# Optimization experiments

Measured on AMD Instinct MI355X. Metric: run time of the kernel, lower is better.

## Reference

```python
import jax, jax.numpy as jnp
import numpy as np

EPS_LN = 1e-5

def _layernorm(x, g, b):
    mu = x.mean(-1, keepdims=True)
    var = ((x - mu) ** 2).mean(-1, keepdims=True)
    return (x - mu) / jnp.sqrt(var + EPS_LN) * g + b


def setup_inputs() -> dict:
    key = jax.random.key(0)
    B, N, D, H = 4, 2048, 256, 4
    hid = int(D * 2.0)
    ks = jax.random.split(key, 12)
    x = jax.random.normal(ks[0], (B, N, D), jnp.float32)
    Au = jax.random.uniform(ks[1], (N, N)) < 0.004
    A = jnp.logical_or(Au, Au.T)
    A = A.at[jnp.arange(N), jnp.arange(N)].set(False)
    Af = A.astype(jnp.float32)
    deg = Af.sum(axis=1)
    L = jnp.diag(deg) - Af                      # graph Laplacian (N,N), PSD
    adjacency = Af + jnp.eye(N, dtype=jnp.float32)  # self loops so no empty softmax rows
    s = lambda k, sh, f: jax.random.normal(k, sh, jnp.float32) * f
    sc = 1.0 / np.sqrt(D)
    Wc = s(ks[2], (D, D), sc); bc = jnp.zeros((D,), jnp.float32)
    Wq = s(ks[3], (D, D), sc); Wk = s(ks[4], (D, D), sc); Wv = s(ks[5], (D, D), sc)
    Wo = s(ks[6], (D, D), sc); bo = jnp.zeros((D,), jnp.float32)
    W1 = s(ks[7], (D, hid), sc); b1 = jnp.zeros((hid,), jnp.float32)
    W2 = s(ks[8], (hid, D), 1.0 / np.sqrt(hid)); b2 = jnp.zeros((D,), jnp.float32)
    g1 = jnp.ones((D,), jnp.float32); be1 = jnp.zeros((D,), jnp.float32)
    g2 = jnp.ones((D,), jnp.float32); be2 = jnp.zeros((D,), jnp.float32)
    g3 = jnp.ones((D,), jnp.float32); be3 = jnp.zeros((D,), jnp.float32)
    return dict(x=x, L=L, adjacency=adjacency, Wc=Wc, bc=bc, g1=g1, be1=be1,
                Wq=Wq, Wk=Wk, Wv=Wv, Wo=Wo, bo=bo, g2=g2, be2=be2,
                W1=W1, b1=b1, W2=W2, b2=b2, g3=g3, be3=be3)


def reference(x, L, adjacency, Wc, bc, g1, be1, Wq, Wk, Wv, Wo, bo,
              g2, be2, W1, b1, W2, b2, g3, be3):
    B, N, D = x.shape
    H = 4
    hd = D // H
    # --- LaplacianConv: normalize L to eigenvalues in [-1, 1] ---
    eig = jnp.linalg.eigvalsh(L)               # ascending
    lam_max = eig[-1] + 1e-8
    L_norm = 2.0 * L / lam_max - jnp.eye(N, dtype=L.dtype)
    # per-channel matmul in torch == single propagation L_norm @ x
    xp = jnp.einsum('mn,bnf->bmf', L_norm, x)
    h = xp @ Wc + bc
    h = _layernorm(h, g1, be1)
    h = jax.nn.relu(h)
    x1 = h + x                                  # residual (in_dim == out_dim)
    # --- adjacency-masked multi-head attention ---
    q = (x1 @ Wq).reshape(B, N, H, hd).transpose(0, 2, 1, 3)  # (B,H,N,hd)
    k = (x1 @ Wk).reshape(B, N, H, hd).transpose(0, 2, 1, 3)
    v = (x1 @ Wv).reshape(B, N, H, hd).transpose(0, 2, 1, 3)
    scores = jnp.einsum('bhnd,bhmd->bhnm', q, k) / np.sqrt(hd).astype(np.float32)
    scores = jnp.where(adjacency[None, None] > 0, scores, jnp.float32(-1e9))
    attn = jax.nn.softmax(scores, axis=-1)
    o = jnp.einsum('bhnm,bhmd->bhnd', attn, v)
    o = o.transpose(0, 2, 1, 3).reshape(B, N, D)
    o = o @ Wo + bo
    x2 = _layernorm(x1 + o, g2, be2)
    # --- MLP ---
    m = jax.nn.gelu(x2 @ W1 + b1, approximate=False) @ W2 + b2
    return _layernorm(x2 + m, g3, be3)
```

## Files before the change

### kernel.cpp

```cpp
#include <hip/hip_runtime.h>
#include <math.h>

typedef __bf16 bf16;
typedef bf16 bf16x8 __attribute__((ext_vector_type(8)));
typedef float f32x4 __attribute__((ext_vector_type(4)));

#define LDS_PAD 40
#define SENT 2048
#define LANCZOS_M 12

__global__ __launch_bounds__(256) void k_pre(
    const float* __restrict__ Wc, const float* __restrict__ Wq, const float* __restrict__ Wk,
    const float* __restrict__ Wv, const float* __restrict__ Wo, const float* __restrict__ W1,
    const float* __restrict__ W2, const float* __restrict__ x, const float* __restrict__ adj,
    bf16* __restrict__ WcT, bf16* __restrict__ WqT, bf16* __restrict__ WkT,
    bf16* __restrict__ WvT, bf16* __restrict__ WoT, bf16* __restrict__ W1T,
    bf16* __restrict__ W2T, bf16* __restrict__ xT,
    int* __restrict__ cnt, unsigned short* __restrict__ cols)
{
    __shared__ float tile[32][33];
    int z = blockIdx.z;
    if (z == 11) {
        int flat = blockIdx.y * 16 + blockIdx.x;
        if (flat >= 512) return;
        int row = flat * 4 + (threadIdx.x >> 6);
        int lane = threadIdx.x & 63;
        int base = 0;
        for (int c0 = 0; c0 < 2048; c0 += 64) {
            float a = adj[(long)row * 2048 + c0 + lane];
            unsigned long long m = __ballot(a != 0.0f);
            if (a != 0.0f) {
                int pos = base + __popcll(m & ((1ull << lane) - 1ull));
                if (pos < 64) cols[(long)row * 64 + pos] = (unsigned short)(c0 + lane);
            }
            base += __popcll(m);
        }
        int c = base < 64 ? base : 64;
        if (lane >= c) cols[(long)row * 64 + lane] = (unsigned short)SENT;
        if (lane == 0) cnt[row] = c;
        return;
    }
    const float* src; bf16* dst; int R, C;
    switch (z) {
        case 0: src = Wc; dst = WcT; R = 256; C = 256; break;
        case 1: src = Wq; dst = WqT; R = 256; C = 256; break;
        case 2: src = Wk; dst = WkT; R = 256; C = 256; break;
        case 3: src = Wv; dst = WvT; R = 256; C = 256; break;
        case 4: src = Wo; dst = WoT; R = 256; C = 256; break;
        case 5: src = W1; dst = W1T; R = 256; C = 512; break;
        case 6: src = W2; dst = W2T; R = 512; C = 256; break;
        default: {
            int b = z - 7;
            src = x + (long)b * 2048 * 256; dst = xT + (long)b * 256 * 2048;
            R = 2048; C = 256;
        }
    }
    int c0 = blockIdx.x * 32, r0 = blockIdx.y * 32;
    if (c0 >= C || r0 >= R) return;
    int tx = threadIdx.x & 31, ty = threadIdx.x >> 5;
#pragma unroll
    for (int j = 0; j < 4; ++j)
        tile[ty + 8 * j][tx] = src[(long)(r0 + ty + 8 * j) * C + c0 + tx];
    __syncthreads();
#pragma unroll
    for (int j = 0; j < 4; ++j)
        dst[(long)(c0 + ty + 8 * j) * R + r0 + tx] = (bf16)tile[tx][ty + 8 * j];
}

__global__ __launch_bounds__(1024) void k_main(
    const int* __restrict__ cnt, const unsigned short* __restrict__ cols, float* __restrict__ lamOut,
    const float* __restrict__ L, const bf16* __restrict__ xT, float* __restrict__ xp0f)
{
    __shared__ float va[2064], vb[2064];
    __shared__ float redf[16], redf2[16];
    __shared__ int   redi[16];
    __shared__ float bcast, bcast2;
    __shared__ float alphaA[LANCZOS_M], betaA[LANCZOS_M];
    __shared__ bf16 As[64 * LDS_PAD];
    __shared__ bf16 Bs[256 * LDS_PAD];

    int t = threadIdx.x;
    if (blockIdx.x != 0) {
        int bx = blockIdx.x - 1;
        int rowBlk = (bx & 31) * 64;
        int z  = (bx >> 5) & 3;
        int ks = bx >> 7;
        long kbase = (long)ks * 1024;
        const bf16* BT = xT + (long)z * 256 * 2048;
        int w = t >> 6, lane = t & 63;
        int q = lane >> 4, l15 = lane & 15;
        int wm = w & 3, wn = w >> 2;

        f32x4 acc[4];
#pragma unroll
        for (int i = 0; i < 4; ++i) acc[i] = (f32x4){0.0f, 0.0f, 0.0f, 0.0f};

        int ar = t >> 4, ac = (t & 15) * 2;
        int br = t >> 2, bc = (t & 3) * 8;
        const float* Ap = L + (long)(rowBlk + ar) * 2048 + kbase + ac;
        const bf16* Bp = BT + (long)br * 2048 + kbase + bc;
        float2 fA = *(const float2*)Ap;
        uint4  rB = *(const uint4*)Bp;
        for (int kt = 0; kt < 1024; kt += 32) {
            __syncthreads();
            {
                union { bf16 h[2]; unsigned u; } pk;
                pk.h[0] = (bf16)fA.x; pk.h[1] = (bf16)fA.y;
                *(unsigned*)&As[ar * LDS_PAD + ac] = pk.u;
            }
            *(uint4*)&Bs[br * LDS_PAD + bc] = rB;
            __syncthreads();
            if (kt + 32 < 1024) {
                fA = *(const float2*)(Ap + kt + 32);
                rB = *(const uint4*)(Bp + kt + 32);
            }
            bf16x8 a = *(const bf16x8*)&As[(wm * 16 + l15) * LDS_PAD + q * 8];
#pragma unroll
            for (int nt = 0; nt < 4; ++nt) {
                bf16x8 b = *(const bf16x8*)&Bs[((wn * 4 + nt) * 16 + l15) * LDS_PAD + q * 8];
                acc[nt] = __builtin_amdgcn_mfma_f32_16x16x32_bf16(a, b, acc[nt], 0, 0, 0);
            }
        }
        long zRow = (long)ks * 8192 + (long)z * 2048 + rowBlk + wm * 16 + q * 4;
#pragma unroll
        for (int nt = 0; nt < 4; ++nt) {
            int col = (wn * 4 + nt) * 16 + l15;
#pragma unroll
            for (int r = 0; r < 4; ++r)
                xp0f[(zRow + r) * 256 + col] = acc[nt][r];
        }
        return;
    }
    int wid = t >> 6, lane = t & 63;
    int r0 = t, r1 = t + 1024;
    int c0 = cnt[r0], c1 = cnt[r1];
    int p0 = (c0 + 7) & ~7, p1 = (c1 + 7) & ~7;

    uint4 cr0[8], cr1[8];
#pragma unroll
    for (int j = 0; j < 8; ++j) {
        cr0[j] = ((const uint4*)(cols + (long)r0 * 64))[j];
        cr1[j] = ((const uint4*)(cols + (long)r1 * 64))[j];
    }

    int md = max(c0, c1);
#pragma unroll
    for (int off = 32; off >= 1; off >>= 1) md = max(md, __shfl_xor(md, off));
    if (lane == 0) redi[wid] = md;
    __syncthreads();
    if (t == 0) {
        int m = 0;
        for (int i = 0; i < 16; ++i) m = max(m, redi[i]);
        bcast = (float)(2 * (m - 1)) + 1.0f;
    }
    for (int i = t; i < 2048; i += 1024) {
        unsigned u = (unsigned)i * 2654435761u;
        u ^= u >> 16; u *= 2246822519u; u ^= u >> 13;
        float mag = 0.5f + (float)((u >> 9) & 1023) * (1.0f / 1024.0f);
        va[i] = (u & 1) ? mag : -mag;
    }
    if (t == 0) { va[SENT] = 0.0f; vb[SENT] = 0.0f; }
    __syncthreads();
    float hiBound = bcast;

    float d0 = va[r0], d1 = va[r1];
    float pz = d0 * d0 + d1 * d1;
#pragma unroll
    for (int off = 32; off >= 1; off >>= 1) pz += __shfl_xor(pz, off);
    if (lane == 0) redf[wid] = pz;
    __syncthreads();
    if (t == 0) { float s = 0; for (int i = 0; i < 16; ++i) s += redf[i]; bcast = s; }
    __syncthreads();
    float sc = rsqrtf(fmaxf(bcast, 1e-30f));
    d0 *= sc; d1 *= sc;
    va[r0] = d0; va[r1] = d1;
    __syncthreads();

    float* cur = va; float* nxt = vb;
    float bp = 0.0f;
    float p0r = 0.0f, p1r = 0.0f;
    for (int it = 0; it < LANCZOS_M; ++it) {
        float sum0 = 0.0f, sum1 = 0.0f;
#pragma unroll
        for (int j = 0; j < 8; ++j)
            if (j * 8 < p0) {
                uint4 q = cr0[j];
                sum0 += cur[q.x & 0xffff] + cur[q.x >> 16] + cur[q.y & 0xffff] + cur[q.y >> 16]
                      + cur[q.z & 0xffff] + cur[q.z >> 16] + cur[q.w & 0xffff] + cur[q.w >> 16];
            }
#pragma unroll
        for (int j = 0; j < 8; ++j)
            if (j * 8 < p1) {
                uint4 q = cr1[j];
                sum1 += cur[q.x & 0xffff] + cur[q.x >> 16] + cur[q.y & 0xffff] + cur[q.y >> 16]
                      + cur[q.z & 0xffff] + cur[q.z >> 16] + cur[q.w & 0xffff] + cur[q.w >> 16];
            }
        float u0 = (float)c0 * d0 - sum0 - bp * p0r;
        float u1 = (float)c1 * d1 - sum1 - bp * p1r;
        float puv = u0 * d0 + u1 * d1;
        float puu = u0 * u0 + u1 * u1;
#pragma unroll
        for (int off = 32; off >= 1; off >>= 1) {
            puv += __shfl_xor(puv, off);
            puu += __shfl_xor(puu, off);
        }
        if (lane == 0) { redf[wid] = puv; redf2[wid] = puu; }
        __syncthreads();
        if (t == 0) {
            float sv = 0, su = 0;
            for (int i = 0; i < 16; ++i) { sv += redf[i]; su += redf2[i]; }
            float b = sqrtf(fmaxf(su - sv * sv, 1e-24f));
            alphaA[it] = sv; betaA[it] = b;
            bcast = sv; bcast2 = b;
        }
        __syncthreads();
        float alpha = bcast, beta = bcast2;
        float invb = 1.0f / beta;
        float w0 = u0 - alpha * d0, w1 = u1 - alpha * d1;
        p0r = d0; p1r = d1;
        d0 = w0 * invb; d1 = w1 * invb;
        nxt[r0] = d0; nxt[r1] = d1;
        __syncthreads();
        bp = beta;
        float* tmp = cur; cur = nxt; nxt = tmp;
    }

    if (t < 64) {
        float aa[LANCZOS_M], b2[LANCZOS_M];
#pragma unroll
        for (int i = 0; i < LANCZOS_M; ++i) { aa[i] = alphaA[i]; b2[i] = betaA[i] * betaA[i]; }
        float lo = 0.0f, hi = hiBound;
        for (int round = 0; round < 4; ++round) {
            float step = (hi - lo) * (1.0f / 65.0f);
            float xm = lo + step * (float)(lane + 1);
            float dd = aa[0] - xm;
            int neg = dd < 0.0f ? 1 : 0;
#pragma unroll
            for (int i = 1; i < LANCZOS_M; ++i) {
                float ad = fmaxf(fabsf(dd), 1e-12f);
                dd = (dd < 0.0f) ? -ad : ad;
                dd = aa[i] - xm - b2[i - 1] / dd;
                neg += dd < 0.0f ? 1 : 0;
            }
            unsigned long long mb = __ballot(neg >= LANCZOS_M);
            if (mb == 0ull) {
                lo = lo + step * 64.0f;
            } else {
                int fl = (int)(__ffsll((long long)mb) - 1);
                hi = lo + step * (float)(fl + 1);
                lo = lo + step * (float)fl;
            }
        }
        if (lane == 0) lamOut[0] = 0.5f * (lo + hi) + 1e-8f;
    }
}

template <int TA, int EPI>
__global__ __launch_bounds__(256) void k_gemm(
    const bf16* __restrict__ A0, const float* __restrict__ Apa, const float* __restrict__ Apb,
    const float* __restrict__ Aaux, const bf16* __restrict__ BTg,
    float* __restrict__ outF, bf16* __restrict__ outB,
    const float* __restrict__ bias, const float* __restrict__ resid,
    const float* __restrict__ gam, const float* __restrict__ bet,
    const float* __restrict__ lamPtr,
    int K, long aZ, long btZ, long outZrows, int ldOut)
{
    __shared__ bf16 As[32 * LDS_PAD];
    __shared__ bf16 Bs[256 * LDS_PAD];
    __shared__ float sL[2][32], sqL[2][32];

    int tid = threadIdx.x;
    int w = tid >> 6, lane = tid & 63;
    int q = lane >> 4, l15 = lane & 15;
    int wm = w & 1, wn = w >> 1;
    int rowBlk = blockIdx.x * 32;
    int colB = blockIdx.y * 256;
    const bf16* BT = BTg + (long)blockIdx.z * btZ + (long)blockIdx.y * 256 * (long)K;

    float s2 = 0.0f;
    if (TA == 2) s2 = 2.0f / lamPtr[0];

    f32x4 acc[8];
#pragma unroll
    for (int i = 0; i < 8; ++i) acc[i] = (f32x4){0.0f, 0.0f, 0.0f, 0.0f};

    int ar = tid >> 3, ac = (tid & 7) * 4;
    long abase = (long)(rowBlk + ar) * K + ac;
    const bf16* A = A0 + (long)blockIdx.z * aZ;
    const bf16* Bp = BT + (long)tid * K;

    uint2 aR;
    float4 pa0, pb0, xa0;
    uint4 bR0, bR1, bR2, bR3;
    if (TA == 1) {
        aR = *(const uint2*)(A + abase);
    } else {
        pa0 = *(const float4*)(Apa + abase);
        pb0 = *(const float4*)(Apb + abase);
        xa0 = *(const float4*)(Aaux + abase);
    }
    bR0 = ((const uint4*)Bp)[0]; bR1 = ((const uint4*)Bp)[1];
    bR2 = ((const uint4*)Bp)[2]; bR3 = ((const uint4*)Bp)[3];

    for (int kt = 0; kt < K; kt += 32) {
        __syncthreads();
        if (TA == 1) {
            *(uint2*)&As[ar * LDS_PAD + ac] = aR;
        } else {
            float pa[4] = {pa0.x, pa0.y, pa0.z, pa0.w};
            float pb[4] = {pb0.x, pb0.y, pb0.z, pb0.w};
            float xa[4] = {xa0.x, xa0.y, xa0.z, xa0.w};
            union { bf16 h[4]; uint2 u; } pk;
#pragma unroll
            for (int j = 0; j < 4; ++j) pk.h[j] = (bf16)(s2 * (pa[j] + pb[j]) - xa[j]);
            *(uint2*)&As[ar * LDS_PAD + ac] = pk.u;
        }
        {
            bf16* d = &Bs[tid * LDS_PAD];
            *(uint4*)(d + 0)  = bR0;
            *(uint4*)(d + 8)  = bR1;
            *(uint4*)(d + 16) = bR2;
            *(uint4*)(d + 24) = bR3;
        }
        __syncthreads();
        if (kt + 32 < K) {
            long nb = abase + kt + 32;
            if (TA == 1) {
                aR = *(const uint2*)(A + nb);
            } else {
                pa0 = *(const float4*)(Apa + nb);
                pb0 = *(const float4*)(Apb + nb);
                xa0 = *(const float4*)(Aaux + nb);
            }
            const bf16* p = Bp + kt + 32;
            bR0 = ((const uint4*)p)[0]; bR1 = ((const uint4*)p)[1];
            bR2 = ((const uint4*)p)[2]; bR3 = ((const uint4*)p)[3];
        }
        bf16x8 a = *(const bf16x8*)&As[(wm * 16 + l15) * LDS_PAD + q * 8];
#pragma unroll
        for (int nt = 0; nt < 8; ++nt) {
            bf16x8 b = *(const bf16x8*)&Bs[((wn * 8 + nt) * 16 + l15) * LDS_PAD + q * 8];
            acc[nt] = __builtin_amdgcn_mfma_f32_16x16x32_bf16(a, b, acc[nt], 0, 0, 0);
        }
    }

    long zRow = (long)blockIdx.z * outZrows + rowBlk + wm * 16 + q * 4;

    if (EPI == 0) {
#pragma unroll
        for (int nt = 0; nt < 8; ++nt) {
            int col = colB + (wn * 8 + nt) * 16 + l15;
#pragma unroll
            for (int r = 0; r < 4; ++r)
                outB[(zRow + r) * (long)ldOut + col] = (bf16)acc[nt][r];
        }
        return;
    }
    if (EPI == 3) {
#pragma unroll
        for (int nt = 0; nt < 8; ++nt) {
            int col = colB + (wn * 8 + nt) * 16 + l15;
            float bi = bias[col];
#pragma unroll
            for (int r = 0; r < 4; ++r) {
                float v = acc[nt][r] + bi;
                float g = 0.5f * v * (1.0f + erff(v * 0.70710678118654752440f));
                outB[(zRow + r) * (long)ldOut + col] = (bf16)g;
            }
        }
        return;
    }
    float s[4] = {0, 0, 0, 0}, sq[4] = {0, 0, 0, 0};
#pragma unroll
    for (int nt = 0; nt < 8; ++nt) {
        int col = colB + (wn * 8 + nt) * 16 + l15;
        float bi = bias[col];
#pragma unroll
        for (int r = 0; r < 4; ++r) {
            float v = acc[nt][r] + bi;
            if (EPI == 2) v += resid[(zRow + r) * 256 + col];
            acc[nt][r] = v;
            s[r] += v; sq[r] += v * v;
        }
    }
#pragma unroll
    for (int off = 1; off <= 8; off <<= 1) {
#pragma unroll
        for (int r = 0; r < 4; ++r) { s[r] += __shfl_xor(s[r], off); sq[r] += __shfl_xor(sq[r], off); }
    }
    if (l15 == 0) {
#pragma unroll
        for (int r = 0; r < 4; ++r) {
            sL[wn][wm * 16 + q * 4 + r] = s[r];
            sqL[wn][wm * 16 + q * 4 + r] = sq[r];
        }
    }
    __syncthreads();
    float mean[4], rstd[4];
#pragma unroll
    for (int r = 0; r < 4; ++r) {
        int row = wm * 16 + q * 4 + r;
        float st = sL[0][row] + sL[1][row];
        float sqt = sqL[0][row] + sqL[1][row];
        mean[r] = st * (1.0f / 256.0f);
        float var = sqt * (1.0f / 256.0f) - mean[r] * mean[r];
        rstd[r] = rsqrtf(var + 1e-5f);
    }
#pragma unroll
    for (int nt = 0; nt < 8; ++nt) {
        int col = colB + (wn * 8 + nt) * 16 + l15;
        float gc = gam[col], bc2 = bet[col];
#pragma unroll
        for (int r = 0; r < 4; ++r) {
            float v = (acc[nt][r] - mean[r]) * rstd[r] * gc + bc2;
            if (EPI == 1) v = fmaxf(v, 0.0f) + resid[(zRow + r) * 256 + col];
            long oi = (zRow + r) * (long)ldOut + col;
            outF[oi] = v;
            if (outB) outB[oi] = (bf16)v;
        }
    }
}

__global__ __launch_bounds__(256) void k_attn(const bf16* __restrict__ qg, const bf16* __restrict__ kg,
                                              const bf16* __restrict__ vg, bf16* __restrict__ og,
                                              const int* __restrict__ cnt, const unsigned short* __restrict__ cols)
{
    __shared__ unsigned short sc[64];
    __shared__ float sp[4][64];
    int row = blockIdx.x;
    int b = row >> 11, i = row & 2047;
    int tid = threadIdx.x, h = tid >> 6, lane = tid & 63;
    int c = cnt[i];
    if (tid < 64) sc[tid] = cols[(long)i * 64 + tid];
    __syncthreads();
    long qoff = (long)row * 256 + h * 64 + lane;
    float qd = (float)qg[qoff];
    long kvBase = (long)b * 2048;
    for (int j = 0; j < c; ++j) {
        int col = sc[j];
        float kd = (float)kg[(kvBase + col) * 256 + h * 64 + lane];
        float p = qd * kd;
#pragma unroll
        for (int off = 32; off >= 1; off >>= 1) p += __shfl_xor(p, off);
        if (lane == 0) sp[h][j] = p * 0.125f;
    }
    __syncthreads();
    float sj = (lane < c) ? sp[h][lane] : -3.0e38f;
    float mx = sj;
#pragma unroll
    for (int off = 32; off >= 1; off >>= 1) mx = fmaxf(mx, __shfl_xor(mx, off));
    float e = (lane < c) ? __expf(sj - mx) : 0.0f;
    float ssum = e;
#pragma unroll
    for (int off = 32; off >= 1; off >>= 1) ssum += __shfl_xor(ssum, off);
    if (lane < c) sp[h][lane] = e / ssum;
    __syncthreads();
    float acc = 0.0f;
    for (int j = 0; j < c; ++j) {
        int col = sc[j];
        acc += sp[h][j] * (float)vg[(kvBase + col) * 256 + h * 64 + lane];
    }
    og[qoff] = (bf16)acc;
}

extern "C" void kernel_launch(void* const* d_in, const int* in_sizes, int n_in,
                              void* d_out, int out_size, void* d_ws, size_t ws_size,
                              hipStream_t stream)
{
    const float* x   = (const float*)d_in[0];
    const float* L   = (const float*)d_in[1];
    const float* adj = (const float*)d_in[2];
    const float* Wc  = (const float*)d_in[3];
    const float* bc  = (const float*)d_in[4];
    const float* g1  = (const float*)d_in[5];
    const float* be1 = (const float*)d_in[6];
    const float* Wq  = (const float*)d_in[7];
    const float* Wk  = (const float*)d_in[8];
    const float* Wv  = (const float*)d_in[9];
    const float* Wo  = (const float*)d_in[10];
    const float* bo  = (const float*)d_in[11];
    const float* g2  = (const float*)d_in[12];
    const float* be2 = (const float*)d_in[13];
    const float* W1  = (const float*)d_in[14];
    const float* b1  = (const float*)d_in[15];
    const float* W2  = (const float*)d_in[16];
    const float* b2  = (const float*)d_in[17];
    const float* g3  = (const float*)d_in[18];
    const float* be3 = (const float*)d_in[19];
    float* out = (float*)d_out;

    char* ws = (char*)d_ws;
    size_t off = 0;
    auto alloc = [&](size_t bytes) -> void* {
        void* p = ws + off;
        off = (off + bytes + 255) & ~(size_t)255;
        return p;
    };
    float* lam           = (float*)alloc(256);
    int* cnt             = (int*)alloc(2048 * 4);
    unsigned short* cols = (unsigned short*)alloc(2048 * 64 * 2);
    bf16* WcT = (bf16*)alloc(65536 * 2);
    bf16* WqT = (bf16*)alloc(65536 * 2);
    bf16* WkT = (bf16*)alloc(65536 * 2);
    bf16* WvT = (bf16*)alloc(65536 * 2);
    bf16* WoT = (bf16*)alloc(65536 * 2);
    bf16* W1T = (bf16*)alloc(131072 * 2);
    bf16* W2T = (bf16*)alloc(131072 * 2);
    bf16* xT  = (bf16*)alloc((size_t)4 * 256 * 2048 * 2);
    float* xp0f = (float*)alloc((size_t)2 * 8192 * 256 * 4);
    float* x1f = (float*)alloc((size_t)8192 * 256 * 4);
    bf16* x1b  = (bf16*)alloc((size_t)8192 * 256 * 2);
    bf16* qb   = (bf16*)alloc((size_t)3 * 8192 * 256 * 2);
    bf16* ob   = (bf16*)alloc((size_t)8192 * 256 * 2);
    float* x2f = (float*)alloc((size_t)8192 * 256 * 4);
    bf16* x2b  = (bf16*)alloc((size_t)8192 * 256 * 2);
    bf16* m1   = (bf16*)alloc((size_t)8192 * 512 * 2);
    (void)in_sizes; (void)n_in; (void)out_size; (void)ws_size;

    dim3 blk(256);
    k_pre<<<dim3(16, 64, 12), blk, 0, stream>>>(Wc, Wq, Wk, Wv, Wo, W1, W2, x, adj,
                                                WcT, WqT, WkT, WvT, WoT, W1T, W2T, xT, cnt, cols);
    k_main<<<dim3(257), dim3(1024), 0, stream>>>(cnt, cols, lam, L, xT, xp0f);
    k_gemm<2, 1><<<dim3(256, 1, 1), blk, 0, stream>>>(
        nullptr, xp0f, xp0f + (size_t)8192 * 256, x, WcT, x1f, x1b, bc, x, g1, be1, lam,
        256, 0L, 0L, 0L, 256);
    k_gemm<1, 0><<<dim3(256, 1, 3), blk, 0, stream>>>(
        x1b, nullptr, nullptr, nullptr, WqT, nullptr, qb, nullptr, nullptr, nullptr, nullptr, nullptr,
        256, 0L, 65536L, 8192L, 256);
    bf16* kb  = qb + (size_t)8192 * 256;
    bf16* vb2 = qb + (size_t)2 * 8192 * 256;
    k_attn<<<dim3(8192), blk, 0, stream>>>(qb, kb, vb2, ob, cnt, cols);
    k_gemm<1, 2><<<dim3(256, 1, 1), blk, 0, stream>>>(
        ob, nullptr, nullptr, nullptr, WoT, x2f, x2b, bo, x1f, g2, be2, nullptr,
        256, 0L, 0L, 0L, 256);
    k_gemm<1, 3><<<dim3(256, 2, 1), blk, 0, stream>>>(
        x2b, nullptr, nullptr, nullptr, W1T, nullptr, m1, b1, nullptr, nullptr, nullptr, nullptr,
        256, 0L, 0L, 0L, 512);
    k_gemm<1, 2><<<dim3(256, 1, 1), blk, 0, stream>>>(
        m1, nullptr, nullptr, nullptr, W2T, out, nullptr, b2, x2f, g3, be3, nullptr,
        512, 0L, 0L, 0L, 256);
}
```

Measured before the change: 368.5 us.

## Fuse GEMM chains into two kernels keeping intermediates in LDS

Replaces the generic templated GEMM launches with two fused kernels. The first computes the Laplacian-conv GEMM with LayerNorm, ReLU and residual, then runs the Q/K/V projections from an LDS-resident x1 tile. The second chains the output projection with LayerNorm, W1 with GELU, and W2 with the final LayerNorm, keeping x2 and the MLP hidden tile in LDS. This removes four launches and the global round-trips for x1b, x2f/x2b and m1. In exchange, the grid for the QKV and W1 stages shrinks from 768/512 blocks to 256, each block does its GEMMs serially, and larger LDS use may lower occupancy.

```diff
diff --git a/kernel.cpp b/kernel.cpp
--- a/kernel.cpp
+++ b/kernel.cpp
@@ -8,6 +8,8 @@
 #define LDS_PAD 40
 #define SENT 2048
 #define LANCZOS_M 12
+#define X1P 264
+#define M1P 520
 
 __global__ __launch_bounds__(256) void k_pre(
     const float* __restrict__ Wc, const float* __restrict__ Wq, const float* __restrict__ Wk,
@@ -255,18 +257,15 @@
     }
 }
 
-template <int TA, int EPI>
-__global__ __launch_bounds__(256) void k_gemm(
-    const bf16* __restrict__ A0, const float* __restrict__ Apa, const float* __restrict__ Apb,
-    const float* __restrict__ Aaux, const bf16* __restrict__ BTg,
-    float* __restrict__ outF, bf16* __restrict__ outB,
-    const float* __restrict__ bias, const float* __restrict__ resid,
-    const float* __restrict__ gam, const float* __restrict__ bet,
-    const float* __restrict__ lamPtr,
-    int K, long aZ, long btZ, long outZrows, int ldOut)
+__global__ __launch_bounds__(256) void k_x1qkv(
+    const float* __restrict__ Apa, const float* __restrict__ Apb, const float* __restrict__ xg,
+    const bf16* __restrict__ WcT, const bf16* __restrict__ WqkvT,
+    const float* __restrict__ bcv, const float* __restrict__ gam, const float* __restrict__ bet,
+    const float* __restrict__ lamPtr, float* __restrict__ x1f, bf16* __restrict__ qkv)
 {
     __shared__ bf16 As[32 * LDS_PAD];
     __shared__ bf16 Bs[256 * LDS_PAD];
+    __shared__ bf16 x1t[32 * X1P];
     __shared__ float sL[2][32], sqL[2][32];
 
     int tid = threadIdx.x;
@@ -274,39 +273,25 @@
     int q = lane >> 4, l15 = lane & 15;
     int wm = w & 1, wn = w >> 1;
     int rowBlk = blockIdx.x * 32;
-    int colB = blockIdx.y * 256;
-    const bf16* BT = BTg + (long)blockIdx.z * btZ + (long)blockIdx.y * 256 * (long)K;
-
-    float s2 = 0.0f;
-    if (TA == 2) s2 = 2.0f / lamPtr[0];
+    float s2 = 2.0f / lamPtr[0];
 
     f32x4 acc[8];
 #pragma unroll
     for (int i = 0; i < 8; ++i) acc[i] = (f32x4){0.0f, 0.0f, 0.0f, 0.0f};
 
     int ar = tid >> 3, ac = (tid & 7) * 4;
-    long abase = (long)(rowBlk + ar) * K + ac;
-    const bf16* A = A0 + (long)blockIdx.z * aZ;
-    const bf16* Bp = BT + (long)tid * K;
-
-    uint2 aR;
-    float4 pa0, pb0, xa0;
-    uint4 bR0, bR1, bR2, bR3;
-    if (TA == 1) {
-        aR = *(const uint2*)(A + abase);
-    } else {
-        pa0 = *(const float4*)(Apa + abase);
-        pb0 = *(const float4*)(Apb + abase);
-        xa0 = *(const float4*)(Aaux + abase);
-    }
-    bR0 = ((const uint4*)Bp)[0]; bR1 = ((const uint4*)Bp)[1];
-    bR2 = ((const uint4*)Bp)[2]; bR3 = ((const uint4*)Bp)[3];
-
-    for (int kt = 0; kt < K; kt += 32) {
-        __syncthreads();
-        if (TA == 1) {
-            *(uint2*)&As[ar * LDS_PAD + ac] = aR;
-        } else {
+    long abase = (long)(rowBlk + ar) * 256 + ac;
+    const bf16* Bp = WcT + (long)tid * 256;
+
+    float4 pa0 = *(const float4*)(Apa + abase);
+    float4 pb0 = *(const float4*)(Apb + abase);
+    float4 xa0 = *(const float4*)(xg + abase);
+    uint4 bR0 = ((const uint4*)Bp)[0], bR1 = ((const uint4*)Bp)[1];
+    uint4 bR2 = ((const uint4*)Bp)[2], bR3 = ((const uint4*)Bp)[3];
+
+    for (int kt = 0; kt < 256; kt += 32) {
+        __syncthreads();
+        {
             float pa[4] = {pa0.x, pa0.y, pa0.z, pa0.w};
             float pb[4] = {pb0.x, pb0.y, pb0.z, pb0.w};
             float xa[4] = {xa0.x, xa0.y, xa0.z, xa0.w};
@@ -323,15 +308,11 @@
             *(uint4*)(d + 24) = bR3;
         }
         __syncthreads();
-        if (kt + 32 < K) {
+        if (kt + 32 < 256) {
             long nb = abase + kt + 32;
-            if (TA == 1) {
-                aR = *(const uint2*)(A + nb);
-            } else {
-                pa0 = *(const float4*)(Apa + nb);
-                pb0 = *(const float4*)(Apb + nb);
-                xa0 = *(const float4*)(Aaux + nb);
-            }
+            pa0 = *(const float4*)(Apa + nb);
+            pb0 = *(const float4*)(Apb + nb);
+            xa0 = *(const float4*)(xg + nb);
             const bf16* p = Bp + kt + 32;
             bR0 = ((const uint4*)p)[0]; bR1 = ((const uint4*)p)[1];
             bR2 = ((const uint4*)p)[2]; bR3 = ((const uint4*)p)[3];
@@ -344,41 +325,15 @@
         }
     }
 
-    long zRow = (long)blockIdx.z * outZrows + rowBlk + wm * 16 + q * 4;
-
-    if (EPI == 0) {
-#pragma unroll
-        for (int nt = 0; nt < 8; ++nt) {
-            int col = colB + (wn * 8 + nt) * 16 + l15;
-#pragma unroll
-            for (int r = 0; r < 4; ++r)
-                outB[(zRow + r) * (long)ldOut + col] = (bf16)acc[nt][r];
-        }
-        return;
-    }
-    if (EPI == 3) {
-#pragma unroll
-        for (int nt = 0; nt < 8; ++nt) {
-            int col = colB + (wn * 8 + nt) * 16 + l15;
-            float bi = bias[col];
-#pragma unroll
-            for (int r = 0; r < 4; ++r) {
-                float v = acc[nt][r] + bi;
-                float g = 0.5f * v * (1.0f + erff(v * 0.70710678118654752440f));
-                outB[(zRow + r) * (long)ldOut + col] = (bf16)g;
-            }
-        }
-        return;
-    }
+    long zRow = (long)rowBlk + wm * 16 + q * 4;
     float s[4] = {0, 0, 0, 0}, sq[4] = {0, 0, 0, 0};
 #pragma unroll
     for (int nt = 0; nt < 8; ++nt) {
-        int col = colB + (wn * 8 + nt) * 16 + l15;
-        float bi = bias[col];
+        int col = (wn * 8 + nt) * 16 + l15;
+        float bi = bcv[col];
 #pragma unroll
         for (int r = 0; r < 4; ++r) {
             float v = acc[nt][r] + bi;
-            if (EPI == 2) v += resid[(zRow + r) * 256 + col];
             acc[nt][r] = v;
             s[r] += v; sq[r] += v * v;
         }
@@ -408,15 +363,285 @@
     }
 #pragma unroll
     for (int nt = 0; nt < 8; ++nt) {
-        int col = colB + (wn * 8 + nt) * 16 + l15;
+        int col = (wn * 8 + nt) * 16 + l15;
         float gc = gam[col], bc2 = bet[col];
 #pragma unroll
         for (int r = 0; r < 4; ++r) {
             float v = (acc[nt][r] - mean[r]) * rstd[r] * gc + bc2;
-            if (EPI == 1) v = fmaxf(v, 0.0f) + resid[(zRow + r) * 256 + col];
-            long oi = (zRow + r) * (long)ldOut + col;
-            outF[oi] = v;
-            if (outB) outB[oi] = (bf16)v;
+            v = fmaxf(v, 0.0f) + xg[(zRow + r) * 256 + col];
+            x1f[(zRow + r) * 256 + col] = v;
+            x1t[(wm * 16 + q * 4 + r) * X1P + col] = (bf16)v;
+        }
+    }
+    __syncthreads();
+
+    for (int z = 0; z < 3; ++z) {
+        const bf16* Bz = WqkvT + (long)z * 65536 + (long)tid * 256;
+        uint4 c0 = ((const uint4*)Bz)[0], c1 = ((const uint4*)Bz)[1];
+        uint4 c2 = ((const uint4*)Bz)[2], c3 = ((const uint4*)Bz)[3];
+        f32x4 a2[8];
+#pragma unroll
+        for (int i = 0; i < 8; ++i) a2[i] = (f32x4){0.0f, 0.0f, 0.0f, 0.0f};
+        for (int kt = 0; kt < 256; kt += 32) {
+            __syncthreads();
+            {
+                bf16* d = &Bs[tid * LDS_PAD];
+                *(uint4*)(d + 0)  = c0;
+                *(uint4*)(d + 8)  = c1;
+                *(uint4*)(d + 16) = c2;
+                *(uint4*)(d + 24) = c3;
+            }
+            __syncthreads();
+            if (kt + 32 < 256) {
+                const bf16* p = Bz + kt + 32;
+                c0 = ((const uint4*)p)[0]; c1 = ((const uint4*)p)[1];
+                c2 = ((const uint4*)p)[2]; c3 = ((const uint4*)p)[3];
+            }
+            bf16x8 a = *(const bf16x8*)&x1t[(wm * 16 + l15) * X1P + kt + q * 8];
+#pragma unroll
+            for (int nt = 0; nt < 8; ++nt) {
+                bf16x8 b = *(const bf16x8*)&Bs[((wn * 8 + nt) * 16 + l15) * LDS_PAD + q * 8];
+                a2[nt] = __builtin_amdgcn_mfma_f32_16x16x32_bf16(a, b, a2[nt], 0, 0, 0);
+            }
+        }
+        bf16* og = qkv + (long)z * 8192 * 256;
+#pragma unroll
+        for (int nt = 0; nt < 8; ++nt) {
+            int col = (wn * 8 + nt) * 16 + l15;
+#pragma unroll
+            for (int r = 0; r < 4; ++r)
+                og[(zRow + r) * 256 + col] = (bf16)a2[nt][r];
+        }
+    }
+}
+
+__global__ __launch_bounds__(256) void k_oW12(
+    const bf16* __restrict__ ob, const bf16* __restrict__ WoT, const float* __restrict__ bo,
+    const float* __restrict__ x1f, const float* __restrict__ g2, const float* __restrict__ be2,
+    const bf16* __restrict__ W1T, const float* __restrict__ b1,
+    const bf16* __restrict__ W2T, const float* __restrict__ b2,
+    const float* __restrict__ g3, const float* __restrict__ be3, float* __restrict__ out)
+{
+    __shared__ bf16 Bs[256 * LDS_PAD];
+    __shared__ bf16 x2t[32 * X1P];
+    __shared__ bf16 m1t[32 * M1P];
+    __shared__ float sL[2][32], sqL[2][32];
+
+    int tid = threadIdx.x;
+    int w = tid >> 6, lane = tid & 63;
+    int q = lane >> 4, l15 = lane & 15;
+    int wm = w & 1, wn = w >> 1;
+    int rowBlk = blockIdx.x * 32;
+    long zRow = (long)rowBlk + wm * 16 + q * 4;
+    bf16* obt = m1t;
+
+    {
+        int row = tid >> 3, coff = (tid & 7) * 32;
+        const bf16* src = ob + (long)(rowBlk + row) * 256 + coff;
+        uint4 u0 = ((const uint4*)src)[0], u1 = ((const uint4*)src)[1];
+        uint4 u2 = ((const uint4*)src)[2], u3 = ((const uint4*)src)[3];
+        bf16* d = &obt[row * X1P + coff];
+        *(uint4*)(d + 0)  = u0;
+        *(uint4*)(d + 8)  = u1;
+        *(uint4*)(d + 16) = u2;
+        *(uint4*)(d + 24) = u3;
+    }
+
+    const bf16* Bp = WoT + (long)tid * 256;
+    uint4 bR0 = ((const uint4*)Bp)[0], bR1 = ((const uint4*)Bp)[1];
+    uint4 bR2 = ((const uint4*)Bp)[2], bR3 = ((const uint4*)Bp)[3];
+    f32x4 acc[8];
+#pragma unroll
+    for (int i = 0; i < 8; ++i) acc[i] = (f32x4){0.0f, 0.0f, 0.0f, 0.0f};
+    for (int kt = 0; kt < 256; kt += 32) {
+        __syncthreads();
+        {
+            bf16* d = &Bs[tid * LDS_PAD];
+            *(uint4*)(d + 0)  = bR0;
+            *(uint4*)(d + 8)  = bR1;
+            *(uint4*)(d + 16) = bR2;
+            *(uint4*)(d + 24) = bR3;
+        }
+        __syncthreads();
+        if (kt + 32 < 256) {
+            const bf16* p = Bp + kt + 32;
+            bR0 = ((const uint4*)p)[0]; bR1 = ((const uint4*)p)[1];
+            bR2 = ((const uint4*)p)[2]; bR3 = ((const uint4*)p)[3];
+        }
+        bf16x8 a = *(const bf16x8*)&obt[(wm * 16 + l15) * X1P + kt + q * 8];
+#pragma unroll
+        for (int nt = 0; nt < 8; ++nt) {
+            bf16x8 b = *(const bf16x8*)&Bs[((wn * 8 + nt) * 16 + l15) * LDS_PAD + q * 8];
+            acc[nt] = __builtin_amdgcn_mfma_f32_16x16x32_bf16(a, b, acc[nt], 0, 0, 0);
+        }
+    }
+    float x2r[8][4];
+    {
+        float s[4] = {0, 0, 0, 0}, sq[4] = {0, 0, 0, 0};
+#pragma unroll
+        for (int nt = 0; nt < 8; ++nt) {
+            int col = (wn * 8 + nt) * 16 + l15;
+            float bi = bo[col];
+#pragma unroll
+            for (int r = 0; r < 4; ++r) {
+                float v = acc[nt][r] + bi + x1f[(zRow + r) * 256 + col];
+                acc[nt][r] = v;
+                s[r] += v; sq[r] += v * v;
+            }
+        }
+#pragma unroll
+        for (int off = 1; off <= 8; off <<= 1) {
+#pragma unroll
+            for (int r = 0; r < 4; ++r) { s[r] += __shfl_xor(s[r], off); sq[r] += __shfl_xor(sq[r], off); }
+        }
+        if (l15 == 0) {
+#pragma unroll
+            for (int r = 0; r < 4; ++r) {
+                sL[wn][wm * 16 + q * 4 + r] = s[r];
+                sqL[wn][wm * 16 + q * 4 + r] = sq[r];
+            }
+        }
+        __syncthreads();
+        float mean[4], rstd[4];
+#pragma unroll
+        for (int r = 0; r < 4; ++r) {
+            int row = wm * 16 + q * 4 + r;
+            float st = sL[0][row] + sL[1][row];
+            float sqt = sqL[0][row] + sqL[1][row];
+            mean[r] = st * (1.0f / 256.0f);
+            float var = sqt * (1.0f / 256.0f) - mean[r] * mean[r];
+            rstd[r] = rsqrtf(var + 1e-5f);
+        }
+#pragma unroll
+        for (int nt = 0; nt < 8; ++nt) {
+            int col = (wn * 8 + nt) * 16 + l15;
+            float gc = g2[col], bc2 = be2[col];
+#pragma unroll
+            for (int r = 0; r < 4; ++r) {
+                float v = (acc[nt][r] - mean[r]) * rstd[r] * gc + bc2;
+                x2r[nt][r] = v;
+                x2t[(wm * 16 + q * 4 + r) * X1P + col] = (bf16)v;
+            }
+        }
+    }
+    __syncthreads();
+
+    for (int cb = 0; cb < 512; cb += 256) {
+        const bf16* B1 = W1T + (long)(cb + tid) * 256;
+        uint4 c0 = ((const uint4*)B1)[0], c1 = ((const uint4*)B1)[1];
+        uint4 c2 = ((const uint4*)B1)[2], c3 = ((const uint4*)B1)[3];
+        f32x4 a2[8];
+#pragma unroll
+        for (int i = 0; i < 8; ++i) a2[i] = (f32x4){0.0f, 0.0f, 0.0f, 0.0f};
+        for (int kt = 0; kt < 256; kt += 32) {
+            __syncthreads();
+            {
+                bf16* d = &Bs[tid * LDS_PAD];
+                *(uint4*)(d + 0)  = c0;
+                *(uint4*)(d + 8)  = c1;
+                *(uint4*)(d + 16) = c2;
+                *(uint4*)(d + 24) = c3;
+            }
+            __syncthreads();
+            if (kt + 32 < 256) {
+                const bf16* p = B1 + kt + 32;
+                c0 = ((const uint4*)p)[0]; c1 = ((const uint4*)p)[1];
+                c2 = ((const uint4*)p)[2]; c3 = ((const uint4*)p)[3];
+            }
+            bf16x8 a = *(const bf16x8*)&x2t[(wm * 16 + l15) * X1P + kt + q * 8];
+#pragma unroll
+            for (int nt = 0; nt < 8; ++nt) {
+                bf16x8 b = *(const bf16x8*)&Bs[((wn * 8 + nt) * 16 + l15) * LDS_PAD + q * 8];
+                a2[nt] = __builtin_amdgcn_mfma_f32_16x16x32_bf16(a, b, a2[nt], 0, 0, 0);
+            }
+        }
+#pragma unroll
+        for (int nt = 0; nt < 8; ++nt) {
+            int col = (wn * 8 + nt) * 16 + l15;
+            float bi = b1[cb + col];
+#pragma unroll
+            for (int r = 0; r < 4; ++r) {
+                float v = a2[nt][r] + bi;
+                float g = 0.5f * v * (1.0f + erff(v * 0.70710678118654752440f));
+                m1t[(wm * 16 + q * 4 + r) * M1P + cb + col] = (bf16)g;
+            }
+        }
+    }
+    __syncthreads();
+
+    const bf16* B2 = W2T + (long)tid * 512;
+    uint4 e0 = ((const uint4*)B2)[0], e1 = ((const uint4*)B2)[1];
+    uint4 e2 = ((const uint4*)B2)[2], e3 = ((const uint4*)B2)[3];
+    f32x4 a3[8];
+#pragma unroll
+    for (int i = 0; i < 8; ++i) a3[i] = (f32x4){0.0f, 0.0f, 0.0f, 0.0f};
+    for (int kt = 0; kt < 512; kt += 32) {
+        __syncthreads();
+        {
+            bf16* d = &Bs[tid * LDS_PAD];
+            *(uint4*)(d + 0)  = e0;
+            *(uint4*)(d + 8)  = e1;
+            *(uint4*)(d + 16) = e2;
+            *(uint4*)(d + 24) = e3;
+        }
+        __syncthreads();
+        if (kt + 32 < 512) {
+            const bf16* p = B2 + kt + 32;
+            e0 = ((const uint4*)p)[0]; e1 = ((const uint4*)p)[1];
+            e2 = ((const uint4*)p)[2]; e3 = ((const uint4*)p)[3];
+        }
+        bf16x8 a = *(const bf16x8*)&m1t[(wm * 16 + l15) * M1P + kt + q * 8];
+#pragma unroll
+        for (int nt = 0; nt < 8; ++nt) {
+            bf16x8 b = *(const bf16x8*)&Bs[((wn * 8 + nt) * 16 + l15) * LDS_PAD + q * 8];
+            a3[nt] = __builtin_amdgcn_mfma_f32_16x16x32_bf16(a, b, a3[nt], 0, 0, 0);
+        }
+    }
+    {
+        float s[4] = {0, 0, 0, 0}, sq[4] = {0, 0, 0, 0};
+#pragma unroll
+        for (int nt = 0; nt < 8; ++nt) {
+            int col = (wn * 8 + nt) * 16 + l15;
+            float bi = b2[col];
+#pragma unroll
+            for (int r = 0; r < 4; ++r) {
+                float v = a3[nt][r] + bi + x2r[nt][r];
+                a3[nt][r] = v;
+                s[r] += v; sq[r] += v * v;
+            }
+        }
+#pragma unroll
+        for (int off = 1; off <= 8; off <<= 1) {
+#pragma unroll
+            for (int r = 0; r < 4; ++r) { s[r] += __shfl_xor(s[r], off); sq[r] += __shfl_xor(sq[r], off); }
+        }
+        if (l15 == 0) {
+#pragma unroll
+            for (int r = 0; r < 4; ++r) {
+                sL[wn][wm * 16 + q * 4 + r] = s[r];
+                sqL[wn][wm * 16 + q * 4 + r] = sq[r];
+            }
+        }
+        __syncthreads();
+        float mean[4], rstd[4];
+#pragma unroll
+        for (int r = 0; r < 4; ++r) {
+            int row = wm * 16 + q * 4 + r;
+            float st = sL[0][row] + sL[1][row];
+            float sqt = sqL[0][row] + sqL[1][row];
+            mean[r] = st * (1.0f / 256.0f);
+            float var = sqt * (1.0f / 256.0f) - mean[r] * mean[r];
+            rstd[r] = rsqrtf(var + 1e-5f);
+        }
+#pragma unroll
+        for (int nt = 0; nt < 8; ++nt) {
+            int col = (wn * 8 + nt) * 16 + l15;
+            float gc = g3[col], bc2 = be3[col];
+#pragma unroll
+            for (int r = 0; r < 4; ++r) {
+                float v = (a3[nt][r] - mean[r]) * rstd[r] * gc + bc2;
+                out[(zRow + r) * 256 + col] = v;
+            }
         }
     }
 }
@@ -509,34 +734,19 @@
     bf16* xT  = (bf16*)alloc((size_t)4 * 256 * 2048 * 2);
     float* xp0f = (float*)alloc((size_t)2 * 8192 * 256 * 4);
     float* x1f = (float*)alloc((size_t)8192 * 256 * 4);
-    bf16* x1b  = (bf16*)alloc((size_t)8192 * 256 * 2);
     bf16* qb   = (bf16*)alloc((size_t)3 * 8192 * 256 * 2);
     bf16* ob   = (bf16*)alloc((size_t)8192 * 256 * 2);
-    float* x2f = (float*)alloc((size_t)8192 * 256 * 4);
-    bf16* x2b  = (bf16*)alloc((size_t)8192 * 256 * 2);
-    bf16* m1   = (bf16*)alloc((size_t)8192 * 512 * 2);
     (void)in_sizes; (void)n_in; (void)out_size; (void)ws_size;
 
     dim3 blk(256);
     k_pre<<<dim3(16, 64, 12), blk, 0, stream>>>(Wc, Wq, Wk, Wv, Wo, W1, W2, x, adj,
                                                 WcT, WqT, WkT, WvT, WoT, W1T, W2T, xT, cnt, cols);
     k_main<<<dim3(257), dim3(1024), 0, stream>>>(cnt, cols, lam, L, xT, xp0f);
-    k_gemm<2, 1><<<dim3(256, 1, 1), blk, 0, stream>>>(
-        nullptr, xp0f, xp0f + (size_t)8192 * 256, x, WcT, x1f, x1b, bc, x, g1, be1, lam,
-        256, 0L, 0L, 0L, 256);
-    k_gemm<1, 0><<<dim3(256, 1, 3), blk, 0, stream>>>(
-        x1b, nullptr, nullptr, nullptr, WqT, nullptr, qb, nullptr, nullptr, nullptr, nullptr, nullptr,
-        256, 0L, 65536L, 8192L, 256);
+    k_x1qkv<<<dim3(256), blk, 0, stream>>>(
+        xp0f, xp0f + (size_t)8192 * 256, x, WcT, WqT, bc, g1, be1, lam, x1f, qb);
     bf16* kb  = qb + (size_t)8192 * 256;
     bf16* vb2 = qb + (size_t)2 * 8192 * 256;
     k_attn<<<dim3(8192), blk, 0, stream>>>(qb, kb, vb2, ob, cnt, cols);
-    k_gemm<1, 2><<<dim3(256, 1, 1), blk, 0, stream>>>(
-        ob, nullptr, nullptr, nullptr, WoT, x2f, x2b, bo, x1f, g2, be2, nullptr,
-        256, 0L, 0L, 0L, 256);
-    k_gemm<1, 3><<<dim3(256, 2, 1), blk, 0, stream>>>(
-        x2b, nullptr, nullptr, nullptr, W1T, nullptr, m1, b1, nullptr, nullptr, nullptr, nullptr,
-        256, 0L, 0L, 0L, 512);
-    k_gemm<1, 2><<<dim3(256, 1, 1), blk, 0, stream>>>(
-        m1, nullptr, nullptr, nullptr, W2T, out, nullptr, b2, x2f, g3, be3, nullptr,
-        512, 0L, 0L, 0L, 256);
+    k_oW12<<<dim3(256), blk, 0, stream>>>(
+        ob, WoT, bo, x1f, g2, be2, W1T, b1, W2T, b2, g3, be3, out);
 }
```

New measurement: 365.9 us. About the same (-0.7%).
